# Kernel tuning notes

Hardware: AMD Instinct MI355X
Metric: run time of the kernel (lower is better)

## Reference

```python
import jax, jax.numpy as jnp
import numpy as np

N_CLASSES = 40
EMBED_DIM = 128
MOMENTUM = 0.1
LAMBDA_R, LAMBDA_C, LAMBDA_M = 1.0, 0.5, 1.0
BATCH = 262144


def setup_inputs() -> dict:
    key = jax.random.key(0)
    k1, k2, k3 = jax.random.split(key, 3)
    z = jax.random.normal(k1, (BATCH, EMBED_DIM), dtype=jnp.float32)
    y = jax.random.randint(k2, (BATCH,), 0, N_CLASSES)
    centers = jax.random.normal(k3, (N_CLASSES, EMBED_DIM), dtype=jnp.float32)
    initialized = jnp.ones((N_CLASSES,), dtype=bool)
    # buffers derived from class_counts (imbalanced ramp), r0=gamma=m0=1, alpha=0.25
    counts = jnp.asarray([1000.0 * (i + 1) for i in range(N_CLASSES)], jnp.float32)
    n_max = jnp.max(counts)
    target_radii = 1.0 + 1.0 * jnp.log(n_max / (counts + 1.0))
    margins = 1.0 * jnp.power(n_max / (counts + 1.0), 0.25)
    return {"z": z, "y": y, "centers": centers, "initialized": initialized,
            "target_radii": target_radii, "margins": margins}


def _update_centers(z, y, centers, initialized):
    # EMA centroid update on detached embeddings (torch.no_grad equivalent).
    zs = jax.lax.stop_gradient(z)
    sums = jax.ops.segment_sum(zs, y, num_segments=N_CLASSES)            # [C, D]
    cnt = jax.ops.segment_sum(jnp.ones((zs.shape[0],), zs.dtype), y,
                              num_segments=N_CLASSES)                    # [C]
    mean = sums / jnp.maximum(cnt, 1.0)[:, None]
    ema = (1.0 - MOMENTUM) * centers + MOMENTUM * mean
    new = jnp.where(initialized[:, None], ema, mean)                     # first-touch init
    return jnp.where((cnt > 0)[:, None], new, centers)                   # skip empty classes


def reference(z, y, centers, initialized, target_radii, margins):
    c = _update_centers(z, y, centers, initialized)                      # [C, D]

    # radial loss: smooth L1 (beta=1) between ||z|| and per-class target radius
    r = jnp.linalg.norm(z, axis=-1)                                      # [B]
    d = r - target_radii[y]
    ad = jnp.abs(d)
    loss_radial = jnp.mean(jnp.where(ad < 1.0, 0.5 * d * d, ad - 0.5))

    # compact loss: mean squared distance to own centroid
    diff = z - c[y]                                                      # [B, D]
    loss_compact = jnp.mean(jnp.sum(diff * diff, axis=-1))

    # margin loss: min distance to any other class centroid via Gram trick
    z2 = jnp.sum(z * z, axis=-1)                                         # [B]
    c2 = jnp.sum(c * c, axis=-1)                                         # [C]
    d2 = z2[:, None] + c2[None, :] - 2.0 * (z @ c.T)                     # [B, C]
    dist = jnp.sqrt(jnp.maximum(d2, 0.0))
    own = y[:, None] == jnp.arange(N_CLASSES)[None, :]                   # [B, C] bool
    dist_opp = jnp.min(jnp.where(own, jnp.inf, dist), axis=1)            # [B]
    loss_margin = jnp.mean(jax.nn.relu(margins[y] - dist_opp))

    return LAMBDA_R * loss_radial + LAMBDA_C * loss_compact + LAMBDA_M * loss_margin
```

## Files before the change

kernel.cpp:

```cpp
#include <hip/hip_runtime.h>
#include <math.h>

#define BATCH 262144
#define DIM   128
#define NCLS  40
#define NCP   48
#define CD    (NCLS * DIM)

#define TB1 512
#define NB1 256
#define TB3 256
#define NB3 (BATCH / 256)

typedef __attribute__((ext_vector_type(8))) short short8;
typedef __attribute__((ext_vector_type(4))) float f32x4;

__device__ __forceinline__ short f2bf(float f) {
    unsigned u = __float_as_uint(f);
    u += 0x7fffu + ((u >> 16) & 1u);
    return (short)(u >> 16);
}

__global__ __launch_bounds__(TB1) void k1_segsum(const float* __restrict__ z,
                                                 const int* __restrict__ y,
                                                 float* __restrict__ part_sums,
                                                 float* __restrict__ gcnt) {
    __shared__ float s_acc[8][NCLS * 64];
    __shared__ float s_cnt[NCLS];
    const int t = threadIdx.x;
    for (int i = t; i < 8 * NCLS * 64; i += TB1) ((float*)s_acc)[i] = 0.0f;
    if (t < NCLS) s_cnt[t] = 0.0f;
    __syncthreads();

    const int w    = t >> 6;
    const int lane = t & 63;
    const int p    = w >> 1;
    const int h    = w & 1;
    const int base = blockIdx.x * 1024;
    float* __restrict__ acc = s_acc[w];

    int yy[4];
#pragma unroll
    for (int g = 0; g < 4; ++g) yy[g] = y[base + 4 * (g * 64 + lane) + p];

    if (h == 0) {
#pragma unroll
        for (int g = 0; g < 4; ++g) atomicAdd(&s_cnt[yy[g]], 1.0f);
    }

    const float* __restrict__ zp = z + (size_t)base * DIM + h * 64 + lane;

    float vb[8];
#pragma unroll
    for (int q = 0; q < 8; ++q) vb[q] = zp[(size_t)(4 * q + p) * DIM];

#pragma unroll 1
    for (int g = 0; g < 4; ++g) {
        const int yg = yy[g];
#pragma unroll
        for (int j0 = 0; j0 < 64; j0 += 8) {
#pragma unroll
            for (int q = 0; q < 8; ++q) {
                const int sj = g * 64 + j0 + q;
                const float v = vb[q];
                int sn = sj + 8;
                if (sn > 255) sn = sj;
                vb[q] = zp[(size_t)(4 * sn + p) * DIM];
                const int cls = __builtin_amdgcn_readlane(yg, j0 + q);
                acc[cls * 64 + lane] += v;
            }
        }
    }
    __syncthreads();

    float* __restrict__ ps = part_sums + (size_t)blockIdx.x * CD;
    for (int i = t; i < CD; i += TB1) {
        const int cls = i >> 7;
        const int d   = i & 127;
        const int hh  = d >> 6, dl = d & 63;
        float ssum = 0.0f;
#pragma unroll
        for (int pp = 0; pp < 4; ++pp) ssum += s_acc[(pp << 1) | hh][cls * 64 + dl];
        ps[i] = ssum;
    }
    if (t < NCLS) atomicAdd(&gcnt[t], s_cnt[t]);
}

__global__ __launch_bounds__(DIM) void k2_centers(const float* __restrict__ part_sums,
                                                  const float* __restrict__ gcnt,
                                                  const float* __restrict__ centers,
                                                  short* __restrict__ cbf,
                                                  float* __restrict__ c2_out) {
    const int j = blockIdx.x;
    const int d = threadIdx.x;

    if (j >= NCLS) {
        cbf[j * DIM + d] = 0;
        if (d == 0) c2_out[j] = 1e30f;
        return;
    }

    const float* __restrict__ p = part_sums + j * DIM + d;
    float s = 0.0f;
#pragma unroll 8
    for (int b = 0; b < NB1; ++b) s += p[(size_t)b * CD];
    const float cnt = gcnt[j];

    const float mean = s / fmaxf(cnt, 1.0f);
    const float ctr  = centers[j * DIM + d];
    const float ema  = 0.9f * ctr + 0.1f * mean;
    const float cv   = (cnt > 0.0f) ? ema : ctr;
    cbf[j * DIM + d] = f2bf(cv);

    __shared__ float red[DIM];
    red[d] = cv * cv;
    __syncthreads();
    for (int off = DIM / 2; off > 0; off >>= 1) {
        if (d < off) red[d] += red[d + off];
        __syncthreads();
    }
    if (d == 0) c2_out[j] = red[0];
}

__global__ __launch_bounds__(TB3) void k3_loss(const float* __restrict__ z,
                                               const int* __restrict__ y,
                                               const short* __restrict__ cbf,
                                               const float* __restrict__ c2,
                                               const float* __restrict__ tr,
                                               const float* __restrict__ mg,
                                               float* __restrict__ partials) {
    __shared__ float s_S[4][64 * 52];
    __shared__ float s_z2[4][64];
    __shared__ float s_c2[NCP];
    __shared__ float s_red[TB3];

    const int t = threadIdx.x;
    if (t < NCP) s_c2[t] = c2[t];

    const int w    = t >> 6;
    const int lane = t & 63;
    const int q    = lane >> 4;
    const int col  = lane & 15;
    const int wavebase = blockIdx.x * 256 + w * 64;

    short8 bfrag[3][4];
#pragma unroll
    for (int ct = 0; ct < 3; ++ct)
#pragma unroll
        for (int s = 0; s < 4; ++s)
            bfrag[ct][s] = *(const short8*)(cbf + (ct * 16 + col) * DIM + s * 32 + q * 8);

    __syncthreads();

#pragma unroll 1
    for (int rt = 0; rt < 4; ++rt) {
        const float* __restrict__ zrow =
            z + (size_t)(wavebase + rt * 16 + col) * DIM + q * 8;

        float4 f[8];
#pragma unroll
        for (int s = 0; s < 4; ++s) {
            f[2 * s]     = *(const float4*)(zrow + s * 32);
            f[2 * s + 1] = *(const float4*)(zrow + s * 32 + 4);
        }

        float zp = 0.0f;
#pragma unroll
        for (int i = 0; i < 8; ++i) {
            zp = fmaf(f[i].x, f[i].x, zp);
            zp = fmaf(f[i].y, f[i].y, zp);
            zp = fmaf(f[i].z, f[i].z, zp);
            zp = fmaf(f[i].w, f[i].w, zp);
        }

        short8 afr[4];
#pragma unroll
        for (int s = 0; s < 4; ++s) {
            const float4 f0 = f[2 * s], f1 = f[2 * s + 1];
            afr[s][0] = f2bf(f0.x); afr[s][1] = f2bf(f0.y);
            afr[s][2] = f2bf(f0.z); afr[s][3] = f2bf(f0.w);
            afr[s][4] = f2bf(f1.x); afr[s][5] = f2bf(f1.y);
            afr[s][6] = f2bf(f1.z); afr[s][7] = f2bf(f1.w);
        }

        f32x4 acc0 = {0.f, 0.f, 0.f, 0.f};
        f32x4 acc1 = {0.f, 0.f, 0.f, 0.f};
        f32x4 acc2 = {0.f, 0.f, 0.f, 0.f};
#pragma unroll
        for (int s = 0; s < 4; ++s) {
            acc0 = __builtin_amdgcn_mfma_f32_16x16x32_bf16(afr[s], bfrag[0][s], acc0, 0, 0, 0);
            acc1 = __builtin_amdgcn_mfma_f32_16x16x32_bf16(afr[s], bfrag[1][s], acc1, 0, 0, 0);
            acc2 = __builtin_amdgcn_mfma_f32_16x16x32_bf16(afr[s], bfrag[2][s], acc2, 0, 0, 0);
        }

        zp += __shfl_xor(zp, 16);
        zp += __shfl_xor(zp, 32);
        if (q == 0) s_z2[w][rt * 16 + col] = zp;

#pragma unroll
        for (int reg = 0; reg < 4; ++reg) {
            const int rr = rt * 16 + q * 4 + reg;
            s_S[w][rr * 52 + col]      = acc0[reg];
            s_S[w][rr * 52 + 16 + col] = acc1[reg];
            s_S[w][rr * 52 + 32 + col] = acc2[reg];
        }
    }

    const int row = blockIdx.x * 256 + t;
    const int cls = y[row];
    const float z2v = s_z2[w][lane];

    float own_d2 = 0.0f;
    float mind2  = 3.4e38f;
#pragma unroll
    for (int k = 0; k < 12; ++k) {
        const float4 Sv = *(const float4*)&s_S[w][lane * 52 + 4 * k];
        const float Se[4] = {Sv.x, Sv.y, Sv.z, Sv.w};
#pragma unroll
        for (int e = 0; e < 4; ++e) {
            const int j = 4 * k + e;
            float d2 = fmaxf(z2v + s_c2[j] - 2.0f * Se[e], 0.0f);
            const bool isown = (j == cls);
            own_d2 = isown ? d2 : own_d2;
            mind2  = isown ? mind2 : fminf(mind2, d2);
        }
    }

    const float r  = sqrtf(z2v);
    const float dd = r - tr[cls];
    const float ad = fabsf(dd);
    const float rad = (ad < 1.0f) ? 0.5f * dd * dd : ad - 0.5f;

    const float dist = sqrtf(mind2);
    const float marg = fmaxf(mg[cls] - dist, 0.0f);

    const float tot = rad + 0.5f * own_d2 + marg;

    s_red[t] = tot;
    __syncthreads();
    for (int off = TB3 / 2; off > 0; off >>= 1) {
        if (t < off) s_red[t] += s_red[t + off];
        __syncthreads();
    }
    if (t == 0) partials[blockIdx.x] = s_red[0];
}

__global__ __launch_bounds__(256) void k4_final(const float* __restrict__ partials,
                                                float* __restrict__ out) {
    __shared__ float sred[256];
    float s = 0.0f;
    for (int i = threadIdx.x; i < NB3; i += 256) s += partials[i];
    sred[threadIdx.x] = s;
    __syncthreads();
    for (int off = 128; off > 0; off >>= 1) {
        if (threadIdx.x < off) sred[threadIdx.x] += sred[threadIdx.x + off];
        __syncthreads();
    }
    if (threadIdx.x == 0) out[0] = sred[0] * (1.0f / (float)BATCH);
}

extern "C" void kernel_launch(void* const* d_in, const int* in_sizes, int n_in,
                              void* d_out, int out_size, void* d_ws, size_t ws_size,
                              hipStream_t stream) {
    const float* z       = (const float*)d_in[0];
    const int*   y       = (const int*)d_in[1];
    const float* centers = (const float*)d_in[2];
    const float* tr      = (const float*)d_in[4];
    const float* mg      = (const float*)d_in[5];
    float* out = (float*)d_out;

    float* ws        = (float*)d_ws;
    float* part_sums = ws;
    float* c2buf     = part_sums + (size_t)NB1 * CD;
    float* gcnt      = c2buf + NCP;
    float* partials  = gcnt + NCLS;
    short* cbf       = (short*)(partials + NB3);

    hipMemsetAsync(gcnt, 0, NCLS * sizeof(float), stream);

    k1_segsum<<<NB1, TB1, 0, stream>>>(z, y, part_sums, gcnt);
    k2_centers<<<NCP, DIM, 0, stream>>>(part_sums, gcnt, centers, cbf, c2buf);
    k3_loss<<<NB3, TB3, 0, stream>>>(z, y, cbf, c2buf, tr, mg, partials);
    k4_final<<<1, 256, 0, stream>>>(partials, out);
}
```

Baseline: 247.2 us.

## Shrink LDS footprints, split center reduction, and fold final reduction into atomics

k1 halves its shared accumulator by having wave pairs share a buffer through LDS atomics. k2 now uses 512 threads so each class's partial-sum reduction is split four ways. k3 drops its separate z2 and reduction buffers by reusing the score tile, adds a 3-blocks-per-CU launch bound, and accumulates the result directly into the output with a global atomic. This removes the final single-block kernel and a launch, but adds LDS and global atomics and makes the float summation order nondeterministic.

```diff
diff --git a/kernel.cpp b/kernel.cpp
--- a/kernel.cpp
+++ b/kernel.cpp
@@ -25,10 +25,10 @@
                                                  const int* __restrict__ y,
                                                  float* __restrict__ part_sums,
                                                  float* __restrict__ gcnt) {
-    __shared__ float s_acc[8][NCLS * 64];
+    __shared__ float s_acc[4][NCLS * 64];
     __shared__ float s_cnt[NCLS];
     const int t = threadIdx.x;
-    for (int i = t; i < 8 * NCLS * 64; i += TB1) ((float*)s_acc)[i] = 0.0f;
+    for (int i = t; i < 4 * NCLS * 64; i += TB1) ((float*)s_acc)[i] = 0.0f;
     if (t < NCLS) s_cnt[t] = 0.0f;
     __syncthreads();
 
@@ -37,7 +37,7 @@
     const int p    = w >> 1;
     const int h    = w & 1;
     const int base = blockIdx.x * 1024;
-    float* __restrict__ acc = s_acc[w];
+    float* __restrict__ acc = s_acc[(p >> 1) * 2 + h];
 
     int yy[4];
 #pragma unroll
@@ -67,7 +67,7 @@
                 if (sn > 255) sn = sj;
                 vb[q] = zp[(size_t)(4 * sn + p) * DIM];
                 const int cls = __builtin_amdgcn_readlane(yg, j0 + q);
-                acc[cls * 64 + lane] += v;
+                atomicAdd(&acc[cls * 64 + lane], v);
             }
         }
     }
@@ -78,61 +78,65 @@
         const int cls = i >> 7;
         const int d   = i & 127;
         const int hh  = d >> 6, dl = d & 63;
-        float ssum = 0.0f;
-#pragma unroll
-        for (int pp = 0; pp < 4; ++pp) ssum += s_acc[(pp << 1) | hh][cls * 64 + dl];
-        ps[i] = ssum;
+        ps[i] = s_acc[hh][cls * 64 + dl] + s_acc[2 + hh][cls * 64 + dl];
     }
     if (t < NCLS) atomicAdd(&gcnt[t], s_cnt[t]);
 }
 
-__global__ __launch_bounds__(DIM) void k2_centers(const float* __restrict__ part_sums,
+__global__ __launch_bounds__(512) void k2_centers(const float* __restrict__ part_sums,
                                                   const float* __restrict__ gcnt,
                                                   const float* __restrict__ centers,
                                                   short* __restrict__ cbf,
                                                   float* __restrict__ c2_out) {
-    const int j = blockIdx.x;
-    const int d = threadIdx.x;
+    const int j  = blockIdx.x;
+    const int t  = threadIdx.x;
+    const int d  = t & 127;
+    const int qr = t >> 7;
 
     if (j >= NCLS) {
-        cbf[j * DIM + d] = 0;
-        if (d == 0) c2_out[j] = 1e30f;
+        if (qr == 0) cbf[j * DIM + d] = 0;
+        if (t == 0) c2_out[j] = 1e30f;
         return;
     }
 
-    const float* __restrict__ p = part_sums + j * DIM + d;
+    const float* __restrict__ p = part_sums + j * DIM + d + (size_t)(qr * 64) * CD;
     float s = 0.0f;
 #pragma unroll 8
-    for (int b = 0; b < NB1; ++b) s += p[(size_t)b * CD];
-    const float cnt = gcnt[j];
-
-    const float mean = s / fmaxf(cnt, 1.0f);
-    const float ctr  = centers[j * DIM + d];
-    const float ema  = 0.9f * ctr + 0.1f * mean;
-    const float cv   = (cnt > 0.0f) ? ema : ctr;
-    cbf[j * DIM + d] = f2bf(cv);
-
-    __shared__ float red[DIM];
-    red[d] = cv * cv;
-    __syncthreads();
-    for (int off = DIM / 2; off > 0; off >>= 1) {
-        if (d < off) red[d] += red[d + off];
+    for (int b = 0; b < 64; ++b) s += p[(size_t)b * CD];
+
+    __shared__ float red[512];
+    red[t] = s;
+    __syncthreads();
+
+    float cv = 0.0f;
+    if (qr == 0) {
+        const float ssum = red[d] + red[d + 128] + red[d + 256] + red[d + 384];
+        const float cnt  = gcnt[j];
+        const float mean = ssum / fmaxf(cnt, 1.0f);
+        const float ctr  = centers[j * DIM + d];
+        const float ema  = 0.9f * ctr + 0.1f * mean;
+        cv = (cnt > 0.0f) ? ema : ctr;
+        cbf[j * DIM + d] = f2bf(cv);
+    }
+    __syncthreads();
+    red[t] = cv * cv;
+    __syncthreads();
+    for (int off = 256; off > 0; off >>= 1) {
+        if (t < off) red[t] += red[t + off];
         __syncthreads();
     }
-    if (d == 0) c2_out[j] = red[0];
-}
-
-__global__ __launch_bounds__(TB3) void k3_loss(const float* __restrict__ z,
-                                               const int* __restrict__ y,
-                                               const short* __restrict__ cbf,
-                                               const float* __restrict__ c2,
-                                               const float* __restrict__ tr,
-                                               const float* __restrict__ mg,
-                                               float* __restrict__ partials) {
+    if (t == 0) c2_out[j] = red[0];
+}
+
+__global__ __launch_bounds__(TB3, 3) void k3_loss(const float* __restrict__ z,
+                                                  const int* __restrict__ y,
+                                                  const short* __restrict__ cbf,
+                                                  const float* __restrict__ c2,
+                                                  const float* __restrict__ tr,
+                                                  const float* __restrict__ mg,
+                                                  float* __restrict__ out) {
     __shared__ float s_S[4][64 * 52];
-    __shared__ float s_z2[4][64];
     __shared__ float s_c2[NCP];
-    __shared__ float s_red[TB3];
 
     const int t = threadIdx.x;
     if (t < NCP) s_c2[t] = c2[t];
@@ -195,7 +199,7 @@
 
         zp += __shfl_xor(zp, 16);
         zp += __shfl_xor(zp, 32);
-        if (q == 0) s_z2[w][rt * 16 + col] = zp;
+        if (q == 0) s_S[w][(rt * 16 + col) * 52 + 48] = zp;
 
 #pragma unroll
         for (int reg = 0; reg < 4; ++reg) {
@@ -208,7 +212,7 @@
 
     const int row = blockIdx.x * 256 + t;
     const int cls = y[row];
-    const float z2v = s_z2[w][lane];
+    const float z2v = s_S[w][lane * 52 + 48];
 
     float own_d2 = 0.0f;
     float mind2  = 3.4e38f;
@@ -236,27 +240,15 @@
 
     const float tot = rad + 0.5f * own_d2 + marg;
 
+    __syncthreads();
+    float* s_red = &s_S[0][0];
     s_red[t] = tot;
     __syncthreads();
     for (int off = TB3 / 2; off > 0; off >>= 1) {
         if (t < off) s_red[t] += s_red[t + off];
         __syncthreads();
     }
-    if (t == 0) partials[blockIdx.x] = s_red[0];
-}
-
-__global__ __launch_bounds__(256) void k4_final(const float* __restrict__ partials,
-                                                float* __restrict__ out) {
-    __shared__ float sred[256];
-    float s = 0.0f;
-    for (int i = threadIdx.x; i < NB3; i += 256) s += partials[i];
-    sred[threadIdx.x] = s;
-    __syncthreads();
-    for (int off = 128; off > 0; off >>= 1) {
-        if (threadIdx.x < off) sred[threadIdx.x] += sred[threadIdx.x + off];
-        __syncthreads();
-    }
-    if (threadIdx.x == 0) out[0] = sred[0] * (1.0f / (float)BATCH);
+    if (t == 0) atomicAdd(out, s_red[0] * (1.0f / (float)BATCH));
 }
 
 extern "C" void kernel_launch(void* const* d_in, const int* in_sizes, int n_in,
@@ -273,13 +265,12 @@
     float* part_sums = ws;
     float* c2buf     = part_sums + (size_t)NB1 * CD;
     float* gcnt      = c2buf + NCP;
-    float* partials  = gcnt + NCLS;
-    short* cbf       = (short*)(partials + NB3);
+    short* cbf       = (short*)(gcnt + NCLS);
 
     hipMemsetAsync(gcnt, 0, NCLS * sizeof(float), stream);
+    hipMemsetAsync(out, 0, sizeof(float), stream);
 
     k1_segsum<<<NB1, TB1, 0, stream>>>(z, y, part_sums, gcnt);
-    k2_centers<<<NCP, DIM, 0, stream>>>(part_sums, gcnt, centers, cbf, c2buf);
-    k3_loss<<<NB3, TB3, 0, stream>>>(z, y, cbf, c2buf, tr, mg, partials);
-    k4_final<<<1, 256, 0, stream>>>(partials, out);
-}
+    k2_centers<<<NCP, 512, 0, stream>>>(part_sums, gcnt, centers, cbf, c2buf);
+    k3_loss<<<NB3, TB3, 0, stream>>>(z, y, cbf, c2buf, tr, mg, out);
+}
```

New measurement: 359.9 us. +45.6%, slower.
